# Optimization experiments

Measured on AMD Instinct MI355X. Metric: run time of the kernel, lower is better.

Reference implementation:

```python
import jax, jax.numpy as jnp
import numpy as np

MAX_LENGTH = 10
SOS = 0


def setup_inputs() -> dict:
    key = jax.random.key(0)
    ks = jax.random.split(key, 16)
    B, S, H, V = 64, 128, 1024, 32000
    sc = 0.02
    return {
        "encoder_outputs": jax.random.normal(ks[0], (B, S, H), jnp.float32),
        "encoder_hidden": jax.random.normal(ks[1], (1, B, H), jnp.float32),
        "target_tensor": jax.random.randint(ks[2], (B, MAX_LENGTH), 0, V),
        "embedding": jax.random.normal(ks[3], (V, H), jnp.float32) * sc,
        "Wa_w": jax.random.normal(ks[4], (H, H), jnp.float32) * sc,
        "Wa_b": jnp.zeros((H,), jnp.float32),
        "Ua_w": jax.random.normal(ks[5], (H, H), jnp.float32) * sc,
        "Ua_b": jnp.zeros((H,), jnp.float32),
        "Va_w": jax.random.normal(ks[6], (1, H), jnp.float32) * sc,
        "Va_b": jnp.zeros((1,), jnp.float32),
        "gru_wi": jax.random.normal(ks[7], (3 * H, 2 * H), jnp.float32) * sc,
        "gru_wh": jax.random.normal(ks[8], (3 * H, H), jnp.float32) * sc,
        "gru_bi": jnp.zeros((3 * H,), jnp.float32),
        "gru_bh": jnp.zeros((3 * H,), jnp.float32),
        "out_w": jax.random.normal(ks[9], (V, H), jnp.float32) * sc,
        "out_b": jnp.zeros((V,), jnp.float32),
    }


def reference(encoder_outputs, encoder_hidden, target_tensor, embedding,
              Wa_w, Wa_b, Ua_w, Ua_b, Va_w, Va_b,
              gru_wi, gru_wh, gru_bi, gru_bh, out_w, out_b):
    B, S, H = encoder_outputs.shape
    # teacher-forced input tokens: [SOS, tgt_0, ..., tgt_{T-2}]
    tokens = jnp.concatenate(
        [jnp.full((B, 1), SOS, dtype=target_tensor.dtype),
         target_tensor[:, :MAX_LENGTH - 1]], axis=1)  # [B, T]
    emb_seq = embedding[tokens]                         # [B, T, H] (dropout = identity)
    # precompute Ua(keys), shared across steps
    Ua_keys = jnp.einsum('bsh,kh->bsk', encoder_outputs, Ua_w) + Ua_b  # [B,S,H]
    va = Va_w[0]

    def step(h, emb_t):  # h: [B,H], emb_t: [B,H]
        q = h @ Wa_w.T + Wa_b                                   # [B,H]
        scores = jnp.einsum('bsh,h->bs', jnp.tanh(q[:, None, :] + Ua_keys), va) + Va_b[0]
        w = jax.nn.softmax(scores, axis=-1)                     # [B,S]
        ctx = jnp.einsum('bs,bsh->bh', w, encoder_outputs)      # [B,H]
        x = jnp.concatenate([emb_t, ctx], axis=-1)              # [B,2H]
        gi = x @ gru_wi.T + gru_bi                              # [B,3H]
        gh = h @ gru_wh.T + gru_bh
        r = jax.nn.sigmoid(gi[:, :H] + gh[:, :H])
        z = jax.nn.sigmoid(gi[:, H:2 * H] + gh[:, H:2 * H])
        n = jnp.tanh(gi[:, 2 * H:] + r * gh[:, 2 * H:])
        h_new = (1.0 - z) * n + z * h
        return h_new, (h_new, w)

    h0 = encoder_hidden[0]  # [B,H]
    h_final, (outs, attns) = jax.lax.scan(step, h0, jnp.swapaxes(emb_seq, 0, 1))
    outs = jnp.swapaxes(outs, 0, 1)                 # [B,T,H]
    attns = jnp.swapaxes(attns, 0, 1)               # [B,T,S]
    logits = jnp.einsum('bth,vh->btv', outs, out_w) + out_b
    log_probs = jax.nn.log_softmax(logits, axis=-1)  # [B,T,V]
    return log_probs, h_final[None], attns
```

## Files before the change

### kernel.cpp

```cpp
#include <hip/hip_runtime.h>
#include <hip/hip_bf16.h>
#include <cstddef>

#define B 64
#define S 128
#define H 1024
#define V 32000
#define T 10
#define H3 3072
#define NCHUNK 250

typedef __bf16 bf16x8 __attribute__((ext_vector_type(8)));
typedef float f32x4 __attribute__((ext_vector_type(4)));
typedef unsigned short ushort8v __attribute__((ext_vector_type(8)));

__device__ inline unsigned short f2b(float f) {
    __hip_bfloat16 h = __float2bfloat16(f);
    return *reinterpret_cast<unsigned short*>(&h);
}
__device__ inline float b2f(unsigned short u) {
    return __uint_as_float(((unsigned)u) << 16);
}
__device__ inline float fast_tanh(float x) {
    float e = __expf(2.f * x);
    return 1.f - 2.f * __builtin_amdgcn_rcpf(e + 1.f);
}
__device__ inline float fast_sigmoid(float x) {
    return __builtin_amdgcn_rcpf(1.f + __expf(-x));
}

__device__ inline void gload_lds16(const void* g, void* l) {
    __builtin_amdgcn_global_load_lds(
        (const __attribute__((address_space(1))) void*)g,
        (__attribute__((address_space(3))) void*)l, 16, 0, 0);
}

__device__ inline int xcd_swz(int orig, int nwg) {
    int q = nwg >> 3, r = nwg & 7;
    int xcd = orig & 7, idx = orig >> 3;
    int base = (xcd < r) ? xcd * (q + 1) : r * (q + 1) + (xcd - r) * q;
    return base + idx;
}

#define PREP_NB 20240
__global__ void prep_kernel(const float* __restrict__ enc, unsigned short* __restrict__ enc_bf,
                            const float* __restrict__ Ua_w, unsigned short* __restrict__ Ua_bf,
                            const float* __restrict__ gwh, const float* __restrict__ Wa_w,
                            unsigned short* __restrict__ Wcat,
                            const float* __restrict__ gwi,
                            unsigned short* __restrict__ Wemb, unsigned short* __restrict__ Wctx,
                            const float* __restrict__ gbh, const float* __restrict__ Wa_b,
                            float* __restrict__ catbias,
                            const float* __restrict__ emb, const int* __restrict__ tgt,
                            unsigned short* __restrict__ embg,
                            const float* __restrict__ h0, unsigned short* __restrict__ hbf,
                            float* __restrict__ hbuf) {
    const int bid = blockIdx.x, tid = threadIdx.x;
    if (bid < 8192) {
        int i = bid * 256 + tid;
        float4 v = reinterpret_cast<const float4*>(enc)[i];
        ushort4 o = { f2b(v.x), f2b(v.y), f2b(v.z), f2b(v.w) };
        reinterpret_cast<ushort4*>(enc_bf)[i] = o;
    } else if (bid < 9216) {
        int i = (bid - 8192) * 256 + tid;
        float4 v = reinterpret_cast<const float4*>(Ua_w)[i];
        ushort4 o = { f2b(v.x), f2b(v.y), f2b(v.z), f2b(v.w) };
        reinterpret_cast<ushort4*>(Ua_bf)[i] = o;
    } else if (bid < 13312) {
        int i = (bid - 9216) * 256 + tid;
        int e = i * 4, n = e >> 10, k = e & 1023;
        const float* src = (n < H3) ? (gwh + (size_t)n * H + k) : (Wa_w + (size_t)(n - H3) * H + k);
        float4 v = *reinterpret_cast<const float4*>(src);
        ushort4 o = { f2b(v.x), f2b(v.y), f2b(v.z), f2b(v.w) };
        reinterpret_cast<ushort4*>(Wcat)[i] = o;
    } else if (bid < 16384) {
        int i = (bid - 13312) * 256 + tid;
        int e = i * 4, n = e >> 10, k = e & 1023;
        float4 v = *reinterpret_cast<const float4*>(gwi + (size_t)n * 2 * H + k);
        ushort4 o = { f2b(v.x), f2b(v.y), f2b(v.z), f2b(v.w) };
        reinterpret_cast<ushort4*>(Wemb)[i] = o;
    } else if (bid < 19456) {
        int i = (bid - 16384) * 256 + tid;
        int e = i * 4, n = e >> 10, k = e & 1023;
        float4 v = *reinterpret_cast<const float4*>(gwi + (size_t)n * 2 * H + H + k);
        ushort4 o = { f2b(v.x), f2b(v.y), f2b(v.z), f2b(v.w) };
        reinterpret_cast<ushort4*>(Wctx)[i] = o;
    } else if (bid < 19472) {
        int n = (bid - 19456) * 256 + tid;
        catbias[n] = (n < H3) ? gbh[n] : Wa_b[n - H3];
    } else if (bid < 20112) {
        int i = (bid - 19472) * 256 + tid;
        int e = i * 4;
        int t = e >> 16, rem = e & 65535;
        int b = rem >> 10, j = rem & 1023;
        int tok = (t == 0) ? 0 : tgt[b * T + (t - 1)];
        float4 v = *reinterpret_cast<const float4*>(emb + (size_t)tok * H + j);
        ushort4 o = { f2b(v.x), f2b(v.y), f2b(v.z), f2b(v.w) };
        *reinterpret_cast<ushort4*>(embg + ((size_t)t * B + b) * H + j) = o;
    } else if (bid < 20176) {
        int i = (bid - 20112) * 256 + tid;
        float4 v = reinterpret_cast<const float4*>(h0)[i];
        ushort4 o = { f2b(v.x), f2b(v.y), f2b(v.z), f2b(v.w) };
        reinterpret_cast<ushort4*>(hbf)[i] = o;
    } else {
        int i = (bid - 20176) * 256 + tid;
        reinterpret_cast<float4*>(hbuf)[i] = reinterpret_cast<const float4*>(h0)[i];
    }
}

struct GemmDesc {
    const unsigned short* A;
    const unsigned short* Bw;
    const float* bias;
    void* C;
    int M, N, out_bf16;
};

__global__ __launch_bounds__(512) void gemm3_kernel(GemmDesc d0, GemmDesc d1, GemmDesc d2,
                                                    const float* __restrict__ out_w,
                                                    unsigned short* __restrict__ outw_bf) {
    __shared__ unsigned short As[128 * 32];
    __shared__ unsigned short Bs[128 * 32];
    const int bid = blockIdx.x;
    const int tid = threadIdx.x;
    if (bid >= 2168) {
        int i = (bid - 2168) * 512 + tid;
        float4 v = reinterpret_cast<const float4*>(out_w)[i];
        ushort4 o = { f2b(v.x), f2b(v.y), f2b(v.z), f2b(v.w) };
        reinterpret_cast<ushort4*>(outw_bf)[i] = o;
        return;
    }
    GemmDesc d; int local, nwg;
    if (bid < 512)       { d = d0; local = bid;        nwg = 512;  }
    else if (bid < 2048) { d = d1; local = bid - 512;  nwg = 1536; }
    else                 { d = d2; local = bid - 2048; nwg = 120;  }
    local = xcd_swz(local, nwg);
    const int mtiles = d.M >> 7;
    const int bm = (local % mtiles) << 7, bn = (local / mtiles) << 7;
    const int lane = tid & 63, w = tid >> 6;
    const int wm = w >> 2, wn = w & 3;
    const int quad = lane >> 4, fr = lane & 15;
    const int K = H;
    f32x4 acc[4][2] = {};

    const int sr = w * 16 + (lane >> 2), sc = (lane & 3) * 8;
    const unsigned short* agp = d.A + (size_t)(bm + sr) * K + sc;
    const unsigned short* bgp = d.Bw + (size_t)(bn + sr) * K + sc;
    unsigned short* alp = As + w * 512;
    unsigned short* blp = Bs + w * 512;

    for (int k0 = 0; k0 < K; k0 += 32) {
        gload_lds16(agp + k0, alp);
        gload_lds16(bgp + k0, blp);
        __syncthreads();
        const int kg = quad * 8;
        bf16x8 a[4], bb[2];
        #pragma unroll
        for (int m = 0; m < 4; ++m)
            a[m] = *reinterpret_cast<const bf16x8*>(&As[(64 * wm + 16 * m + fr) * 32 + kg]);
        #pragma unroll
        for (int n = 0; n < 2; ++n)
            bb[n] = *reinterpret_cast<const bf16x8*>(&Bs[(32 * wn + 16 * n + fr) * 32 + kg]);
        #pragma unroll
        for (int m = 0; m < 4; ++m)
            #pragma unroll
            for (int n = 0; n < 2; ++n)
                acc[m][n] = __builtin_amdgcn_mfma_f32_16x16x32_bf16(a[m], bb[n], acc[m][n], 0, 0, 0);
        __syncthreads();
    }
    #pragma unroll
    for (int n = 0; n < 2; ++n) {
        int col = bn + 32 * wn + 16 * n + fr;
        float bv = d.bias ? d.bias[col] : 0.f;
        #pragma unroll
        for (int m = 0; m < 4; ++m)
            #pragma unroll
            for (int i = 0; i < 4; ++i) {
                int row = bm + 64 * wm + 16 * m + quad * 4 + i;
                float v = acc[m][n][i] + bv;
                if (d.out_bf16)
                    ((unsigned short*)d.C)[(size_t)row * d.N + col] = f2b(v);
                else
                    ((float*)d.C)[(size_t)row * d.N + col] = v;
            }
    }
}

__global__ __launch_bounds__(512) void gemm_logits(const unsigned short* __restrict__ A,
                                                   const unsigned short* __restrict__ Bw,
                                                   const float* __restrict__ bias,
                                                   float* __restrict__ Cout,
                                                   float2* __restrict__ stats,
                                                   int M, int N, int K) {
    __shared__ unsigned short As[128 * 32];
    __shared__ unsigned short Bs[128 * 32];
    __shared__ float mred[128][4];
    __shared__ float sred[128][4];
    const int wg = xcd_swz(blockIdx.x, gridDim.x);
    const int mtiles = M >> 7;
    const int bm = (wg % mtiles) << 7, bn = (wg / mtiles) << 7;
    const int tid = threadIdx.x, lane = tid & 63, w = tid >> 6;
    const int wm = w >> 2, wn = w & 3;
    const int quad = lane >> 4, fr = lane & 15;
    f32x4 acc[4][2] = {};

    const int sr = w * 16 + (lane >> 2), sc = (lane & 3) * 8;
    const unsigned short* agp = A + (size_t)(bm + sr) * K + sc;
    const unsigned short* bgp = Bw + (size_t)(bn + sr) * K + sc;
    unsigned short* alp = As + w * 512;
    unsigned short* blp = Bs + w * 512;

    for (int k0 = 0; k0 < K; k0 += 32) {
        gload_lds16(agp + k0, alp);
        gload_lds16(bgp + k0, blp);
        __syncthreads();
        const int kg = quad * 8;
        bf16x8 a[4], bb[2];
        #pragma unroll
        for (int m = 0; m < 4; ++m)
            a[m] = *reinterpret_cast<const bf16x8*>(&As[(64 * wm + 16 * m + fr) * 32 + kg]);
        #pragma unroll
        for (int n = 0; n < 2; ++n)
            bb[n] = *reinterpret_cast<const bf16x8*>(&Bs[(32 * wn + 16 * n + fr) * 32 + kg]);
        #pragma unroll
        for (int m = 0; m < 4; ++m)
            #pragma unroll
            for (int n = 0; n < 2; ++n)
                acc[m][n] = __builtin_amdgcn_mfma_f32_16x16x32_bf16(a[m], bb[n], acc[m][n], 0, 0, 0);
        __syncthreads();
    }

    #pragma unroll
    for (int n = 0; n < 2; ++n) {
        int col = bn + 32 * wn + 16 * n + fr;
        float bv = bias[col];
        #pragma unroll
        for (int m = 0; m < 4; ++m)
            #pragma unroll
            for (int i = 0; i < 4; ++i) {
                int row = bm + 64 * wm + 16 * m + quad * 4 + i;
                float v = acc[m][n][i] + bv;
                Cout[(size_t)row * N + col] = v;
                acc[m][n][i] = v;
            }
    }

    const int nchunk = N >> 7;
    #pragma unroll
    for (int m = 0; m < 4; ++m)
        #pragma unroll
        for (int i = 0; i < 4; ++i) {
            float x = fmaxf(acc[m][0][i], acc[m][1][i]);
            x = fmaxf(x, __shfl_xor(x, 1)); x = fmaxf(x, __shfl_xor(x, 2));
            x = fmaxf(x, __shfl_xor(x, 4)); x = fmaxf(x, __shfl_xor(x, 8));
            if (fr == 0) mred[64 * wm + 16 * m + quad * 4 + i][wn] = x;
        }
    __syncthreads();
    #pragma unroll
    for (int m = 0; m < 4; ++m)
        #pragma unroll
        for (int i = 0; i < 4; ++i) {
            int rl = 64 * wm + 16 * m + quad * 4 + i;
            float Mr = fmaxf(fmaxf(mred[rl][0], mred[rl][1]), fmaxf(mred[rl][2], mred[rl][3]));
            float sv = expf(acc[m][0][i] - Mr) + expf(acc[m][1][i] - Mr);
            sv += __shfl_xor(sv, 1); sv += __shfl_xor(sv, 2);
            sv += __shfl_xor(sv, 4); sv += __shfl_xor(sv, 8);
            if (fr == 0) sred[rl][wn] = sv;
        }
    __syncthreads();
    if (tid < 128) {
        float Mr = fmaxf(fmaxf(mred[tid][0], mred[tid][1]), fmaxf(mred[tid][2], mred[tid][3]));
        float Sv = sred[tid][0] + sred[tid][1] + sred[tid][2] + sred[tid][3];
        stats[(size_t)(bm + tid) * nchunk + (bn >> 7)] = make_float2(Mr, Sv);
    }
}

__global__ __launch_bounds__(256) void gemm_smallA(const unsigned short* __restrict__ A,
                                                   const unsigned short* __restrict__ Bw,
                                                   const float* __restrict__ bias,
                                                   float* __restrict__ Cout) {
    __shared__ unsigned short As[64][136];
    __shared__ unsigned short Bs[32][136];
    const int bn = blockIdx.x * 32;
    const int tid = threadIdx.x, lane = tid & 63, w = tid >> 6;
    const int quad = lane >> 4, fr = lane & 15;
    f32x4 acc[2] = {};

    const int srA = tid >> 2, scA = (tid & 3) * 32;
    const int srB = tid >> 3, scB = (tid & 7) * 16;
    for (int k0 = 0; k0 < H; k0 += 128) {
        const unsigned short* ap = A + (size_t)srA * H + k0 + scA;
        #pragma unroll
        for (int u = 0; u < 4; ++u)
            *reinterpret_cast<bf16x8*>(&As[srA][scA + 8 * u]) =
                *reinterpret_cast<const bf16x8*>(ap + 8 * u);
        const unsigned short* bp = Bw + (size_t)(bn + srB) * H + k0 + scB;
        *reinterpret_cast<bf16x8*>(&Bs[srB][scB])     = *reinterpret_cast<const bf16x8*>(bp);
        *reinterpret_cast<bf16x8*>(&Bs[srB][scB + 8]) = *reinterpret_cast<const bf16x8*>(bp + 8);
        __syncthreads();
        #pragma unroll
        for (int ks = 0; ks < 4; ++ks) {
            const int kg = quad * 8 + 32 * ks;
            bf16x8 a = *reinterpret_cast<const bf16x8*>(&As[16 * w + fr][kg]);
            #pragma unroll
            for (int n = 0; n < 2; ++n) {
                bf16x8 bb = *reinterpret_cast<const bf16x8*>(&Bs[16 * n + fr][kg]);
                acc[n] = __builtin_amdgcn_mfma_f32_16x16x32_bf16(a, bb, acc[n], 0, 0, 0);
            }
        }
        __syncthreads();
    }
    #pragma unroll
    for (int n = 0; n < 2; ++n) {
        int col = bn + 16 * n + fr;
        float bv = bias[col];
        #pragma unroll
        for (int i = 0; i < 4; ++i) {
            int row = 16 * w + quad * 4 + i;
            Cout[(size_t)row * 4096 + col] = acc[n][i] + bv;
        }
    }
}

__global__ __launch_bounds__(256) void stepB(const float* __restrict__ ghq,
                                             const unsigned short* __restrict__ keys,
                                             const unsigned short* __restrict__ KV,
                                             const float* __restrict__ va,
                                             const float* __restrict__ va_b,
                                             const float* __restrict__ gi_emb,
                                             float* __restrict__ h,
                                             unsigned short* __restrict__ hbf,
                                             unsigned short* __restrict__ outs_bf,
                                             float* __restrict__ attns,
                                             float* __restrict__ h_final, int t) {
    const int q = blockIdx.x, b = blockIdx.y;
    const int tid = threadIdx.x, lane = tid & 63, wv = tid >> 6;
    __shared__ float ssc[128];
    __shared__ float sw[128];
    __shared__ float red[4][64][13];

    float qv[16], vv[16];
    {
        const float* qp = ghq + (size_t)b * 4096 + H3 + lane * 16;
        const float* vp = va + lane * 16;
        #pragma unroll
        for (int j = 0; j < 16; ++j) { qv[j] = qp[j]; vv[j] = vp[j]; }
    }
    const float vab = va_b[0];
    const unsigned short* kb = keys + (size_t)b * S * H;
    for (int i = 0; i < 32; i += 2) {
        int s0 = wv * 32 + i;
        const unsigned short* kr0 = kb + (size_t)s0 * H + lane * 16;
        const unsigned short* kr1 = kr0 + H;
        ushort8v k00 = *reinterpret_cast<const ushort8v*>(kr0);
        ushort8v k01 = *reinterpret_cast<const ushort8v*>(kr0 + 8);
        ushort8v k10 = *reinterpret_cast<const ushort8v*>(kr1);
        ushort8v k11 = *reinterpret_cast<const ushort8v*>(kr1 + 8);
        float a0 = 0.f, a1 = 0.f;
        #pragma unroll
        for (int e = 0; e < 8; ++e) {
            a0 += fast_tanh(qv[e] + b2f(k00[e])) * vv[e];
            a1 += fast_tanh(qv[e] + b2f(k10[e])) * vv[e];
        }
        #pragma unroll
        for (int e = 0; e < 8; ++e) {
            a0 += fast_tanh(qv[8 + e] + b2f(k01[e])) * vv[8 + e];
            a1 += fast_tanh(qv[8 + e] + b2f(k11[e])) * vv[8 + e];
        }
        a0 += __shfl_xor(a0, 1);  a1 += __shfl_xor(a1, 1);
        a0 += __shfl_xor(a0, 2);  a1 += __shfl_xor(a1, 2);
        a0 += __shfl_xor(a0, 4);  a1 += __shfl_xor(a1, 4);
        a0 += __shfl_xor(a0, 8);  a1 += __shfl_xor(a1, 8);
        a0 += __shfl_xor(a0, 16); a1 += __shfl_xor(a1, 16);
        a0 += __shfl_xor(a0, 32); a1 += __shfl_xor(a1, 32);
        if (lane == 0) { ssc[s0] = a0 + vab; ssc[s0 + 1] = a1 + vab; }
    }
    __syncthreads();
    if (tid < 128) {
        float mx = -1e30f;
        #pragma unroll 8
        for (int s = 0; s < 128; ++s) mx = fmaxf(mx, ssc[s]);
        float sum = 0.f;
        #pragma unroll 8
        for (int s = 0; s < 128; ++s) sum += __expf(ssc[s] - mx);
        float wvv = __expf(ssc[tid] - mx) / sum;
        sw[tid] = wvv;
        if (q == 0) attns[((size_t)b * T + t) * S + tid] = wvv;
    }
    __syncthreads();

    const int j0 = q * 256 + lane * 4;
    float ar[4] = {}, az[4] = {}, an[4] = {};
    const unsigned short* kvb = KV + (size_t)b * S * H3 + j0;
    for (int i = 0; i < 32; i += 2) {
        int s0 = wv * 32 + i;
        float w0 = sw[s0], w1 = sw[s0 + 1];
        const unsigned short* r0 = kvb + (size_t)s0 * H3;
        const unsigned short* r1 = r0 + H3;
        uint2 u0a = *reinterpret_cast<const uint2*>(r0);
        uint2 u1a = *reinterpret_cast<const uint2*>(r0 + 1024);
        uint2 u2a = *reinterpret_cast<const uint2*>(r0 + 2048);
        uint2 u0b = *reinterpret_cast<const uint2*>(r1);
        uint2 u1b = *reinterpret_cast<const uint2*>(r1 + 1024);
        uint2 u2b = *reinterpret_cast<const uint2*>(r1 + 2048);
        ar[0] += w0 * b2f((unsigned short)(u0a.x & 0xffff)) + w1 * b2f((unsigned short)(u0b.x & 0xffff));
        ar[1] += w0 * b2f((unsigned short)(u0a.x >> 16))    + w1 * b2f((unsigned short)(u0b.x >> 16));
        ar[2] += w0 * b2f((unsigned short)(u0a.y & 0xffff)) + w1 * b2f((unsigned short)(u0b.y & 0xffff));
        ar[3] += w0 * b2f((unsigned short)(u0a.y >> 16))    + w1 * b2f((unsigned short)(u0b.y >> 16));
        az[0] += w0 * b2f((unsigned short)(u1a.x & 0xffff)) + w1 * b2f((unsigned short)(u1b.x & 0xffff));
        az[1] += w0 * b2f((unsigned short)(u1a.x >> 16))    + w1 * b2f((unsigned short)(u1b.x >> 16));
        az[2] += w0 * b2f((unsigned short)(u1a.y & 0xffff)) + w1 * b2f((unsigned short)(u1b.y & 0xffff));
        az[3] += w0 * b2f((unsigned short)(u1a.y >> 16))    + w1 * b2f((unsigned short)(u1b.y >> 16));
        an[0] += w0 * b2f((unsigned short)(u2a.x & 0xffff)) + w1 * b2f((unsigned short)(u2b.x & 0xffff));
        an[1] += w0 * b2f((unsigned short)(u2a.x >> 16))    + w1 * b2f((unsigned short)(u2b.x >> 16));
        an[2] += w0 * b2f((unsigned short)(u2a.y & 0xffff)) + w1 * b2f((unsigned short)(u2b.y & 0xffff));
        an[3] += w0 * b2f((unsigned short)(u2a.y >> 16))    + w1 * b2f((unsigned short)(u2b.y >> 16));
    }
    #pragma unroll
    for (int g = 0; g < 4; ++g) {
        red[wv][lane][g]     = ar[g];
        red[wv][lane][4 + g] = az[g];
        red[wv][lane][8 + g] = an[g];
    }
    __syncthreads();

    if (tid < 64) {
        float rr[4], zz[4], nn[4];
        #pragma unroll
        for (int g = 0; g < 4; ++g) {
            rr[g] = red[0][tid][g] + red[1][tid][g] + red[2][tid][g] + red[3][tid][g];
            zz[g] = red[0][tid][4+g] + red[1][tid][4+g] + red[2][tid][4+g] + red[3][tid][4+g];
            nn[g] = red[0][tid][8+g] + red[1][tid][8+g] + red[2][tid][8+g] + red[3][tid][8+g];
        }
        const int jj = q * 256 + tid * 4;
        const float* ge = gi_emb + ((size_t)t * B + b) * H3;
        const float* gh = ghq + (size_t)b * 4096;
        float geR[4], geZ[4], geN[4], ghR[4], ghZ[4], ghN[4], hv[4];
        *reinterpret_cast<float4*>(geR) = *reinterpret_cast<const float4*>(ge + jj);
        *reinterpret_cast<float4*>(geZ) = *reinterpret_cast<const float4*>(ge + 1024 + jj);
        *reinterpret_cast<float4*>(geN) = *reinterpret_cast<const float4*>(ge + 2048 + jj);
        *reinterpret_cast<float4*>(ghR) = *reinterpret_cast<const float4*>(gh + jj);
        *reinterpret_cast<float4*>(ghZ) = *reinterpret_cast<const float4*>(gh + 1024 + jj);
        *reinterpret_cast<float4*>(ghN) = *reinterpret_cast<const float4*>(gh + 2048 + jj);
        *reinterpret_cast<float4*>(hv)  = *reinterpret_cast<const float4*>(h + (size_t)b * H + jj);
        ushort4 hb;
        unsigned short* hbp = reinterpret_cast<unsigned short*>(&hb);
        #pragma unroll
        for (int i = 0; i < 4; ++i) {
            float r = fast_sigmoid(geR[i] + rr[i] + ghR[i]);
            float z = fast_sigmoid(geZ[i] + zz[i] + ghZ[i]);
            float n = fast_tanh(geN[i] + nn[i] + r * ghN[i]);
            hv[i] = (1.f - z) * n + z * hv[i];
            hbp[i] = f2b(hv[i]);
        }
        *reinterpret_cast<float4*>(h + (size_t)b * H + jj) = *reinterpret_cast<float4*>(hv);
        *reinterpret_cast<ushort4*>(hbf + (size_t)b * H + jj) = hb;
        *reinterpret_cast<ushort4*>(outs_bf + ((size_t)b * T + t) * H + jj) = hb;
        if (t == T - 1)
            *reinterpret_cast<float4*>(h_final + (size_t)b * H + jj) = *reinterpret_cast<float4*>(hv);
    }
}

__global__ void lsesub_kernel(const float2* __restrict__ stats, float* __restrict__ x) {
    const int row = blockIdx.x;
    const int tid = threadIdx.x;
    __shared__ float shm[256];
    __shared__ float shs[256];
    float mv = -1e30f, sv = 0.f;
    float2 st = make_float2(-1e30f, 0.f);
    if (tid < NCHUNK) { st = stats[(size_t)row * NCHUNK + tid]; mv = st.x; }
    shm[tid] = mv; __syncthreads();
    for (int off = 128; off > 0; off >>= 1) {
        if (tid < off) shm[tid] = fmaxf(shm[tid], shm[tid + off]);
        __syncthreads();
    }
    float M = shm[0]; __syncthreads();
    if (tid < NCHUNK) sv = st.y * expf(st.x - M);
    shs[tid] = sv; __syncthreads();
    for (int off = 128; off > 0; off >>= 1) {
        if (tid < off) shs[tid] += shs[tid + off];
        __syncthreads();
    }
    float L = M + logf(shs[0]);
    __syncthreads();
    float4* p = reinterpret_cast<float4*>(x + (size_t)row * V);
    for (int i = tid; i < V / 4; i += 256) {
        float4 v = p[i];
        v.x -= L; v.y -= L; v.z -= L; v.w -= L;
        p[i] = v;
    }
}


extern "C" void kernel_launch(void* const* d_in, const int* in_sizes, int n_in,
                              void* d_out, int out_size, void* d_ws, size_t ws_size,
                              hipStream_t stream) {
    const float* enc   = (const float*)d_in[0];
    const float* h0    = (const float*)d_in[1];
    const int*   tgt   = (const int*)d_in[2];
    const float* emb   = (const float*)d_in[3];
    const float* Wa_w  = (const float*)d_in[4];
    const float* Wa_b  = (const float*)d_in[5];
    const float* Ua_w  = (const float*)d_in[6];
    const float* Ua_b  = (const float*)d_in[7];
    const float* Va_w  = (const float*)d_in[8];
    const float* Va_b  = (const float*)d_in[9];
    const float* gwi   = (const float*)d_in[10];
    const float* gwh   = (const float*)d_in[11];
    const float* gbi   = (const float*)d_in[12];
    const float* gbh   = (const float*)d_in[13];
    const float* out_w = (const float*)d_in[14];
    const float* out_b = (const float*)d_in[15];

    float* out       = (float*)d_out;
    float* log_probs = out;
    float* h_final   = out + (size_t)B * T * V;
    float* attns     = h_final + (size_t)B * H;

    char* pp = (char*)d_ws;
    auto alloc = [&](size_t bytes) { char* r = pp; pp += (bytes + 255) & ~(size_t)255; return r; };
    unsigned short* ua_bf   = (unsigned short*)alloc((size_t)B * S * H * 2);
    unsigned short* enc_bf  = (unsigned short*)alloc((size_t)B * S * H * 2);
    unsigned short* outw_bf = (unsigned short*)alloc((size_t)V * H * 2);
    unsigned short* KV      = (unsigned short*)alloc((size_t)B * S * H3 * 2);
    unsigned short* Ua_bf   = (unsigned short*)alloc((size_t)H * H * 2);
    unsigned short* Wcat    = (unsigned short*)alloc((size_t)4096 * H * 2);
    unsigned short* Wctx    = (unsigned short*)alloc((size_t)H3 * H * 2);
    unsigned short* Wemb    = (unsigned short*)alloc((size_t)H3 * H * 2);
    float*          catbias = (float*)alloc(4096 * 4);
    unsigned short* embg    = (unsigned short*)alloc((size_t)T * B * H * 2);
    float*          gi_emb  = (float*)alloc((size_t)T * B * H3 * 4);
    float*          hbuf    = (float*)alloc((size_t)B * H * 4);
    unsigned short* hbf     = (unsigned short*)alloc((size_t)B * H * 2);
    float*          ghq     = (float*)alloc((size_t)B * 4096 * 4);
    unsigned short* outs_bf = (unsigned short*)alloc((size_t)B * T * H * 2);
    float2*         stats   = (float2*)alloc((size_t)B * T * NCHUNK * 8);

    prep_kernel<<<PREP_NB, 256, 0, stream>>>(enc, enc_bf, Ua_w, Ua_bf,
                                             gwh, Wa_w, Wcat, gwi, Wemb, Wctx,
                                             gbh, Wa_b, catbias, emb, tgt, embg,
                                             h0, hbf, hbuf);

    GemmDesc d0 = { enc_bf, Ua_bf, Ua_b, (void*)ua_bf,  B * S, H,  1 };
    GemmDesc d1 = { enc_bf, Wctx,  nullptr, (void*)KV,  B * S, H3, 1 };
    GemmDesc d2 = { embg,   Wemb,  gbi, (void*)gi_emb,  T * B, H3, 0 };
    gemm3_kernel<<<18168, 512, 0, stream>>>(d0, d1, d2, out_w, outw_bf);

    for (int t = 0; t < T; ++t) {
        gemm_smallA<<<128, 256, 0, stream>>>(hbf, Wcat, catbias, ghq);
        stepB<<<dim3(4, B), 256, 0, stream>>>(ghq, ua_bf, KV, Va_w, Va_b, gi_emb,
                                              hbuf, hbf, outs_bf, attns, h_final, t);
    }

    gemm_logits<<<(B * T / 128) * (V / 128), 512, 0, stream>>>(
        outs_bf, outw_bf, out_b, log_probs, stats, B * T, V, H);
    lsesub_kernel<<<B * T, 256, 0, stream>>>(stats, log_probs);
}
```

Before: 712.3 us.

## Fuse per-step GEMM and attention/GRU kernels with atomic-counter grid handoff

Merges the small hidden-state GEMM and the attention/GRU step into one launch per timestep. The first 128 blocks compute ghq and bump per-group atomic counters. The remaining 256 blocks spin on a completion counter before reading ghq. This removes one kernel launch and its inter-kernel gap per step, at the cost of spin-waiting and relying on all blocks being co-resident. It also adds a memset of the per-step counters.

```diff
diff --git a/kernel.cpp b/kernel.cpp
--- a/kernel.cpp
+++ b/kernel.cpp
@@ -275,70 +275,85 @@
     }
 }
 
-__global__ __launch_bounds__(256) void gemm_smallA(const unsigned short* __restrict__ A,
-                                                   const unsigned short* __restrict__ Bw,
-                                                   const float* __restrict__ bias,
-                                                   float* __restrict__ Cout) {
-    __shared__ unsigned short As[64][136];
-    __shared__ unsigned short Bs[32][136];
-    const int bn = blockIdx.x * 32;
-    const int tid = threadIdx.x, lane = tid & 63, w = tid >> 6;
+__global__ __launch_bounds__(256) void step_kernel(const unsigned short* __restrict__ hbf_in,
+                                                   const unsigned short* __restrict__ Wcat,
+                                                   const float* __restrict__ catbias,
+                                                   float* __restrict__ ghq,
+                                                   const unsigned short* __restrict__ keys,
+                                                   const unsigned short* __restrict__ KV,
+                                                   const float* __restrict__ va,
+                                                   const float* __restrict__ va_b,
+                                                   const float* __restrict__ gi_emb,
+                                                   float* __restrict__ h,
+                                                   unsigned short* __restrict__ hbf_out,
+                                                   unsigned short* __restrict__ outs_bf,
+                                                   float* __restrict__ attns,
+                                                   float* __restrict__ h_final,
+                                                   unsigned int* __restrict__ ctr, int t) {
+    const int bid = blockIdx.x;
+    const int tid = threadIdx.x, lane = tid & 63, wv = tid >> 6;
     const int quad = lane >> 4, fr = lane & 15;
-    f32x4 acc[2] = {};
-
-    const int srA = tid >> 2, scA = (tid & 3) * 32;
-    const int srB = tid >> 3, scB = (tid & 7) * 16;
-    for (int k0 = 0; k0 < H; k0 += 128) {
-        const unsigned short* ap = A + (size_t)srA * H + k0 + scA;
-        #pragma unroll
-        for (int u = 0; u < 4; ++u)
-            *reinterpret_cast<bf16x8*>(&As[srA][scA + 8 * u]) =
-                *reinterpret_cast<const bf16x8*>(ap + 8 * u);
-        const unsigned short* bp = Bw + (size_t)(bn + srB) * H + k0 + scB;
-        *reinterpret_cast<bf16x8*>(&Bs[srB][scB])     = *reinterpret_cast<const bf16x8*>(bp);
-        *reinterpret_cast<bf16x8*>(&Bs[srB][scB + 8]) = *reinterpret_cast<const bf16x8*>(bp + 8);
-        __syncthreads();
-        #pragma unroll
-        for (int ks = 0; ks < 4; ++ks) {
-            const int kg = quad * 8 + 32 * ks;
-            bf16x8 a = *reinterpret_cast<const bf16x8*>(&As[16 * w + fr][kg]);
-            #pragma unroll
-            for (int n = 0; n < 2; ++n) {
-                bf16x8 bb = *reinterpret_cast<const bf16x8*>(&Bs[16 * n + fr][kg]);
-                acc[n] = __builtin_amdgcn_mfma_f32_16x16x32_bf16(a, bb, acc[n], 0, 0, 0);
+
+    if (bid < 128) {
+        __shared__ unsigned short As[64][136];
+        __shared__ unsigned short Bs[32][136];
+        const int bn = bid * 32;
+        f32x4 acc[2] = {};
+        const int srA = tid >> 2, scA = (tid & 3) * 32;
+        const int srB = tid >> 3, scB = (tid & 7) * 16;
+        for (int k0 = 0; k0 < H; k0 += 128) {
+            const unsigned short* ap = hbf_in + (size_t)srA * H + k0 + scA;
+            #pragma unroll
+            for (int u = 0; u < 4; ++u)
+                *reinterpret_cast<bf16x8*>(&As[srA][scA + 8 * u]) =
+                    *reinterpret_cast<const bf16x8*>(ap + 8 * u);
+            const unsigned short* bp = Wcat + (size_t)(bn + srB) * H + k0 + scB;
+            *reinterpret_cast<bf16x8*>(&Bs[srB][scB])     = *reinterpret_cast<const bf16x8*>(bp);
+            *reinterpret_cast<bf16x8*>(&Bs[srB][scB + 8]) = *reinterpret_cast<const bf16x8*>(bp + 8);
+            __syncthreads();
+            #pragma unroll
+            for (int ks = 0; ks < 4; ++ks) {
+                const int kg = quad * 8 + 32 * ks;
+                bf16x8 a = *reinterpret_cast<const bf16x8*>(&As[16 * wv + fr][kg]);
+                #pragma unroll
+                for (int n = 0; n < 2; ++n) {
+                    bf16x8 bb = *reinterpret_cast<const bf16x8*>(&Bs[16 * n + fr][kg]);
+                    acc[n] = __builtin_amdgcn_mfma_f32_16x16x32_bf16(a, bb, acc[n], 0, 0, 0);
+                }
             }
-        }
-        __syncthreads();
-    }
-    #pragma unroll
-    for (int n = 0; n < 2; ++n) {
-        int col = bn + 16 * n + fr;
-        float bv = bias[col];
-        #pragma unroll
-        for (int i = 0; i < 4; ++i) {
-            int row = 16 * w + quad * 4 + i;
-            Cout[(size_t)row * 4096 + col] = acc[n][i] + bv;
-        }
-    }
-}
-
-__global__ __launch_bounds__(256) void stepB(const float* __restrict__ ghq,
-                                             const unsigned short* __restrict__ keys,
-                                             const unsigned short* __restrict__ KV,
-                                             const float* __restrict__ va,
-                                             const float* __restrict__ va_b,
-                                             const float* __restrict__ gi_emb,
-                                             float* __restrict__ h,
-                                             unsigned short* __restrict__ hbf,
-                                             unsigned short* __restrict__ outs_bf,
-                                             float* __restrict__ attns,
-                                             float* __restrict__ h_final, int t) {
-    const int q = blockIdx.x, b = blockIdx.y;
-    const int tid = threadIdx.x, lane = tid & 63, wv = tid >> 6;
+            __syncthreads();
+        }
+        #pragma unroll
+        for (int n = 0; n < 2; ++n) {
+            int col = bn + 16 * n + fr;
+            float bv = catbias[col];
+            #pragma unroll
+            for (int i = 0; i < 4; ++i) {
+                int row = 16 * wv + quad * 4 + i;
+                ghq[(size_t)row * 4096 + col] = acc[n][i] + bv;
+            }
+        }
+        __syncthreads();
+        if (tid == 0) {
+            __threadfence();
+            unsigned old = atomicAdd(&ctr[(bid >> 5) * 32], 1u);
+            if (old == 31u) atomicAdd(&ctr[4 * 32], 1u);
+        }
+        return;
+    }
+
     __shared__ float ssc[128];
     __shared__ float sw[128];
     __shared__ float red[4][64][13];
-
+    if (tid == 0) {
+        while (__hip_atomic_load(&ctr[4 * 32], __ATOMIC_RELAXED, __HIP_MEMORY_SCOPE_AGENT) < 4u)
+            __builtin_amdgcn_s_sleep(2);
+        __builtin_amdgcn_fence(__ATOMIC_ACQUIRE, "agent");
+    }
+    __syncthreads();
+
+    const int bid2 = bid - 128;
+    const int q = bid2 & 3, b = bid2 >> 2;
     float qv[16], vv[16];
     {
         const float* qp = ghq + (size_t)b * 4096 + H3 + lane * 16;
@@ -454,7 +469,7 @@
             hbp[i] = f2b(hv[i]);
         }
         *reinterpret_cast<float4*>(h + (size_t)b * H + jj) = *reinterpret_cast<float4*>(hv);
-        *reinterpret_cast<ushort4*>(hbf + (size_t)b * H + jj) = hb;
+        *reinterpret_cast<ushort4*>(hbf_out + (size_t)b * H + jj) = hb;
         *reinterpret_cast<ushort4*>(outs_bf + ((size_t)b * T + t) * H + jj) = hb;
         if (t == T - 1)
             *reinterpret_cast<float4*>(h_final + (size_t)b * H + jj) = *reinterpret_cast<float4*>(hv);
@@ -535,6 +550,9 @@
     float*          ghq     = (float*)alloc((size_t)B * 4096 * 4);
     unsigned short* outs_bf = (unsigned short*)alloc((size_t)B * T * H * 2);
     float2*         stats   = (float2*)alloc((size_t)B * T * NCHUNK * 8);
+    unsigned int*   ctrs    = (unsigned int*)alloc((size_t)T * 5 * 32 * 4);
+
+    hipMemsetAsync(ctrs, 0, (size_t)T * 5 * 32 * 4, stream);
 
     prep_kernel<<<PREP_NB, 256, 0, stream>>>(enc, enc_bf, Ua_w, Ua_bf,
                                              gwh, Wa_w, Wcat, gwi, Wemb, Wctx,
@@ -547,9 +565,9 @@
     gemm3_kernel<<<18168, 512, 0, stream>>>(d0, d1, d2, out_w, outw_bf);
 
     for (int t = 0; t < T; ++t) {
-        gemm_smallA<<<128, 256, 0, stream>>>(hbf, Wcat, catbias, ghq);
-        stepB<<<dim3(4, B), 256, 0, stream>>>(ghq, ua_bf, KV, Va_w, Va_b, gi_emb,
-                                              hbuf, hbf, outs_bf, attns, h_final, t);
+        step_kernel<<<384, 256, 0, stream>>>(hbf, Wcat, catbias, ghq, ua_bf, KV,
+                                             Va_w, Va_b, gi_emb, hbuf, hbf, outs_bf,
+                                             attns, h_final, ctrs + (size_t)t * 5 * 32, t);
     }
 
     gemm_logits<<<(B * T / 128) * (V / 128), 512, 0, stream>>>(
```

Result: slower. 780.2 us (+9.5%).

## Fuse fp32-to-bf16 conversion into precompute GEMM loads and drop prep kernel

Applied to the files above, without the earlier changes.

Removes the separate prep kernel that converted encoder outputs and weights to bf16. The precompute GEMMs now read fp32 operands directly, convert them in registers, and store them to LDS. The embedding gather is folded into the A-row addressing, and the remaining small conversions move into spare blocks of the GEMM launch. The GEMM K-step also doubles to 64 using two LDS buffers, halving barrier count. This saves one launch and the bf16 intermediate round-trips through memory. The cost is fp32 global loads, which are twice as wide, plus conversion work inside the GEMM, and the direct global-to-LDS path is dropped for this kernel.

```diff
diff --git a/kernel.cpp b/kernel.cpp
--- a/kernel.cpp
+++ b/kernel.cpp
@@ -42,94 +42,71 @@
     return base + idx;
 }
 
-#define PREP_NB 20240
-__global__ void prep_kernel(const float* __restrict__ enc, unsigned short* __restrict__ enc_bf,
-                            const float* __restrict__ Ua_w, unsigned short* __restrict__ Ua_bf,
-                            const float* __restrict__ gwh, const float* __restrict__ Wa_w,
-                            unsigned short* __restrict__ Wcat,
-                            const float* __restrict__ gwi,
-                            unsigned short* __restrict__ Wemb, unsigned short* __restrict__ Wctx,
-                            const float* __restrict__ gbh, const float* __restrict__ Wa_b,
-                            float* __restrict__ catbias,
-                            const float* __restrict__ emb, const int* __restrict__ tgt,
-                            unsigned short* __restrict__ embg,
-                            const float* __restrict__ h0, unsigned short* __restrict__ hbf,
-                            float* __restrict__ hbuf) {
-    const int bid = blockIdx.x, tid = threadIdx.x;
-    if (bid < 8192) {
-        int i = bid * 256 + tid;
-        float4 v = reinterpret_cast<const float4*>(enc)[i];
-        ushort4 o = { f2b(v.x), f2b(v.y), f2b(v.z), f2b(v.w) };
-        reinterpret_cast<ushort4*>(enc_bf)[i] = o;
-    } else if (bid < 9216) {
-        int i = (bid - 8192) * 256 + tid;
-        float4 v = reinterpret_cast<const float4*>(Ua_w)[i];
-        ushort4 o = { f2b(v.x), f2b(v.y), f2b(v.z), f2b(v.w) };
-        reinterpret_cast<ushort4*>(Ua_bf)[i] = o;
-    } else if (bid < 13312) {
-        int i = (bid - 9216) * 256 + tid;
-        int e = i * 4, n = e >> 10, k = e & 1023;
-        const float* src = (n < H3) ? (gwh + (size_t)n * H + k) : (Wa_w + (size_t)(n - H3) * H + k);
-        float4 v = *reinterpret_cast<const float4*>(src);
-        ushort4 o = { f2b(v.x), f2b(v.y), f2b(v.z), f2b(v.w) };
-        reinterpret_cast<ushort4*>(Wcat)[i] = o;
-    } else if (bid < 16384) {
-        int i = (bid - 13312) * 256 + tid;
-        int e = i * 4, n = e >> 10, k = e & 1023;
-        float4 v = *reinterpret_cast<const float4*>(gwi + (size_t)n * 2 * H + k);
-        ushort4 o = { f2b(v.x), f2b(v.y), f2b(v.z), f2b(v.w) };
-        reinterpret_cast<ushort4*>(Wemb)[i] = o;
-    } else if (bid < 19456) {
-        int i = (bid - 16384) * 256 + tid;
-        int e = i * 4, n = e >> 10, k = e & 1023;
-        float4 v = *reinterpret_cast<const float4*>(gwi + (size_t)n * 2 * H + H + k);
-        ushort4 o = { f2b(v.x), f2b(v.y), f2b(v.z), f2b(v.w) };
-        reinterpret_cast<ushort4*>(Wctx)[i] = o;
-    } else if (bid < 19472) {
-        int n = (bid - 19456) * 256 + tid;
-        catbias[n] = (n < H3) ? gbh[n] : Wa_b[n - H3];
-    } else if (bid < 20112) {
-        int i = (bid - 19472) * 256 + tid;
-        int e = i * 4;
-        int t = e >> 16, rem = e & 65535;
-        int b = rem >> 10, j = rem & 1023;
-        int tok = (t == 0) ? 0 : tgt[b * T + (t - 1)];
-        float4 v = *reinterpret_cast<const float4*>(emb + (size_t)tok * H + j);
-        ushort4 o = { f2b(v.x), f2b(v.y), f2b(v.z), f2b(v.w) };
-        *reinterpret_cast<ushort4*>(embg + ((size_t)t * B + b) * H + j) = o;
-    } else if (bid < 20176) {
-        int i = (bid - 20112) * 256 + tid;
-        float4 v = reinterpret_cast<const float4*>(h0)[i];
-        ushort4 o = { f2b(v.x), f2b(v.y), f2b(v.z), f2b(v.w) };
-        reinterpret_cast<ushort4*>(hbf)[i] = o;
-    } else {
-        int i = (bid - 20176) * 256 + tid;
-        reinterpret_cast<float4*>(hbuf)[i] = reinterpret_cast<const float4*>(h0)[i];
-    }
-}
-
+__device__ inline ushort8v cvt8(const float* p) {
+    float4 f0 = *reinterpret_cast<const float4*>(p);
+    float4 f1 = *reinterpret_cast<const float4*>(p + 4);
+    ushort8v u;
+    u[0] = f2b(f0.x); u[1] = f2b(f0.y); u[2] = f2b(f0.z); u[3] = f2b(f0.w);
+    u[4] = f2b(f1.x); u[5] = f2b(f1.y); u[6] = f2b(f1.z); u[7] = f2b(f1.w);
+    return u;
+}
+
+#define G3_NB 20288
 struct GemmDesc {
-    const unsigned short* A;
-    const unsigned short* Bw;
+    const float* A;
+    const float* Bw;
     const float* bias;
     void* C;
-    int M, N, out_bf16;
+    int M, N;
+    int brstride, bcoff;
+    int out_bf16, gatherA;
 };
 
 __global__ __launch_bounds__(512) void gemm3_kernel(GemmDesc d0, GemmDesc d1, GemmDesc d2,
+                                                    const int* __restrict__ tgt,
                                                     const float* __restrict__ out_w,
-                                                    unsigned short* __restrict__ outw_bf) {
-    __shared__ unsigned short As[128 * 32];
-    __shared__ unsigned short Bs[128 * 32];
+                                                    unsigned short* __restrict__ outw_bf,
+                                                    const float* __restrict__ gwh,
+                                                    const float* __restrict__ Wa_w,
+                                                    unsigned short* __restrict__ Wcat,
+                                                    const float* __restrict__ gbh,
+                                                    const float* __restrict__ Wa_b,
+                                                    float* __restrict__ catbias,
+                                                    const float* __restrict__ h0,
+                                                    unsigned short* __restrict__ hbf,
+                                                    float* __restrict__ hbuf) {
     const int bid = blockIdx.x;
     const int tid = threadIdx.x;
     if (bid >= 2168) {
-        int i = (bid - 2168) * 512 + tid;
-        float4 v = reinterpret_cast<const float4*>(out_w)[i];
-        ushort4 o = { f2b(v.x), f2b(v.y), f2b(v.z), f2b(v.w) };
-        reinterpret_cast<ushort4*>(outw_bf)[i] = o;
+        if (bid < 18168) {
+            int i = (bid - 2168) * 512 + tid;
+            float4 v = reinterpret_cast<const float4*>(out_w)[i];
+            ushort4 o = { f2b(v.x), f2b(v.y), f2b(v.z), f2b(v.w) };
+            reinterpret_cast<ushort4*>(outw_bf)[i] = o;
+        } else if (bid < 20216) {
+            int i = (bid - 18168) * 512 + tid;
+            int e = i * 4, n = e >> 10, k = e & 1023;
+            const float* src = (n < H3) ? (gwh + (size_t)n * H + k) : (Wa_w + (size_t)(n - H3) * H + k);
+            float4 v = *reinterpret_cast<const float4*>(src);
+            ushort4 o = { f2b(v.x), f2b(v.y), f2b(v.z), f2b(v.w) };
+            reinterpret_cast<ushort4*>(Wcat)[i] = o;
+        } else if (bid < 20224) {
+            int n = (bid - 20216) * 512 + tid;
+            catbias[n] = (n < H3) ? gbh[n] : Wa_b[n - H3];
+        } else if (bid < 20256) {
+            int i = (bid - 20224) * 512 + tid;
+            float4 v = reinterpret_cast<const float4*>(h0)[i];
+            ushort4 o = { f2b(v.x), f2b(v.y), f2b(v.z), f2b(v.w) };
+            reinterpret_cast<ushort4*>(hbf)[i] = o;
+        } else {
+            int i = (bid - 20256) * 512 + tid;
+            reinterpret_cast<float4*>(hbuf)[i] = reinterpret_cast<const float4*>(h0)[i];
+        }
         return;
     }
+
+    __shared__ unsigned short As0[128 * 32], As1[128 * 32];
+    __shared__ unsigned short Bs0[128 * 32], Bs1[128 * 32];
     GemmDesc d; int local, nwg;
     if (bid < 512)       { d = d0; local = bid;        nwg = 512;  }
     else if (bid < 2048) { d = d1; local = bid - 512;  nwg = 1536; }
@@ -140,32 +117,53 @@
     const int lane = tid & 63, w = tid >> 6;
     const int wm = w >> 2, wn = w & 3;
     const int quad = lane >> 4, fr = lane & 15;
-    const int K = H;
     f32x4 acc[4][2] = {};
 
-    const int sr = w * 16 + (lane >> 2), sc = (lane & 3) * 8;
-    const unsigned short* agp = d.A + (size_t)(bm + sr) * K + sc;
-    const unsigned short* bgp = d.Bw + (size_t)(bn + sr) * K + sc;
-    unsigned short* alp = As + w * 512;
-    unsigned short* blp = Bs + w * 512;
-
-    for (int k0 = 0; k0 < K; k0 += 32) {
-        gload_lds16(agp + k0, alp);
-        gload_lds16(bgp + k0, blp);
-        __syncthreads();
-        const int kg = quad * 8;
-        bf16x8 a[4], bb[2];
-        #pragma unroll
-        for (int m = 0; m < 4; ++m)
-            a[m] = *reinterpret_cast<const bf16x8*>(&As[(64 * wm + 16 * m + fr) * 32 + kg]);
-        #pragma unroll
-        for (int n = 0; n < 2; ++n)
-            bb[n] = *reinterpret_cast<const bf16x8*>(&Bs[(32 * wn + 16 * n + fr) * 32 + kg]);
-        #pragma unroll
-        for (int m = 0; m < 4; ++m)
+    const int sr = tid >> 2, q4 = tid & 3;
+    const int ck = q4 >> 1, cc = (q4 & 1) * 16;
+    const int gcol = ck * 32 + cc;
+    unsigned short* asel = (ck ? As1 : As0) + sr * 32 + cc;
+    unsigned short* bsel = (ck ? Bs1 : Bs0) + sr * 32 + cc;
+
+    const float* arow;
+    if (d.gatherA) {
+        int m = bm + sr;
+        int tt = m >> 6, bb = m & 63;
+        int tok = (tt == 0) ? 0 : tgt[bb * T + tt - 1];
+        arow = d.A + (size_t)tok * H;
+    } else {
+        arow = d.A + (size_t)(bm + sr) * H;
+    }
+    const float* brow = d.Bw + (size_t)(bn + sr) * d.brstride + d.bcoff;
+
+    for (int k0 = 0; k0 < H; k0 += 64) {
+        ushort8v ua0 = cvt8(arow + k0 + gcol);
+        ushort8v ua1 = cvt8(arow + k0 + gcol + 8);
+        ushort8v ub0 = cvt8(brow + k0 + gcol);
+        ushort8v ub1 = cvt8(brow + k0 + gcol + 8);
+        *reinterpret_cast<ushort8v*>(asel)     = ua0;
+        *reinterpret_cast<ushort8v*>(asel + 8) = ua1;
+        *reinterpret_cast<ushort8v*>(bsel)     = ub0;
+        *reinterpret_cast<ushort8v*>(bsel + 8) = ub1;
+        __syncthreads();
+        #pragma unroll
+        for (int ks = 0; ks < 2; ++ks) {
+            const unsigned short* Asrc = ks ? As1 : As0;
+            const unsigned short* Bsrc = ks ? Bs1 : Bs0;
+            const int kg = quad * 8;
+            bf16x8 a[4], bb[2];
+            #pragma unroll
+            for (int m = 0; m < 4; ++m)
+                a[m] = *reinterpret_cast<const bf16x8*>(&Asrc[(64 * wm + 16 * m + fr) * 32 + kg]);
             #pragma unroll
             for (int n = 0; n < 2; ++n)
-                acc[m][n] = __builtin_amdgcn_mfma_f32_16x16x32_bf16(a[m], bb[n], acc[m][n], 0, 0, 0);
+                bb[n] = *reinterpret_cast<const bf16x8*>(&Bsrc[(32 * wn + 16 * n + fr) * 32 + kg]);
+            #pragma unroll
+            for (int m = 0; m < 4; ++m)
+                #pragma unroll
+                for (int n = 0; n < 2; ++n)
+                    acc[m][n] = __builtin_amdgcn_mfma_f32_16x16x32_bf16(a[m], bb[n], acc[m][n], 0, 0, 0);
+        }
         __syncthreads();
     }
     #pragma unroll
@@ -192,8 +190,8 @@
                                                    float* __restrict__ Cout,
                                                    float2* __restrict__ stats,
                                                    int M, int N, int K) {
-    __shared__ unsigned short As[128 * 32];
-    __shared__ unsigned short Bs[128 * 32];
+    __shared__ unsigned short As0[128 * 32], As1[128 * 32];
+    __shared__ unsigned short Bs0[128 * 32], Bs1[128 * 32];
     __shared__ float mred[128][4];
     __shared__ float sred[128][4];
     const int wg = xcd_swz(blockIdx.x, gridDim.x);
@@ -207,26 +205,35 @@
     const int sr = w * 16 + (lane >> 2), sc = (lane & 3) * 8;
     const unsigned short* agp = A + (size_t)(bm + sr) * K + sc;
     const unsigned short* bgp = Bw + (size_t)(bn + sr) * K + sc;
-    unsigned short* alp = As + w * 512;
-    unsigned short* blp = Bs + w * 512;
-
-    for (int k0 = 0; k0 < K; k0 += 32) {
-        gload_lds16(agp + k0, alp);
-        gload_lds16(bgp + k0, blp);
-        __syncthreads();
-        const int kg = quad * 8;
-        bf16x8 a[4], bb[2];
-        #pragma unroll
-        for (int m = 0; m < 4; ++m)
-            a[m] = *reinterpret_cast<const bf16x8*>(&As[(64 * wm + 16 * m + fr) * 32 + kg]);
-        #pragma unroll
-        for (int n = 0; n < 2; ++n)
-            bb[n] = *reinterpret_cast<const bf16x8*>(&Bs[(32 * wn + 16 * n + fr) * 32 + kg]);
-        #pragma unroll
-        for (int m = 0; m < 4; ++m)
+    unsigned short* a0 = As0 + w * 512;
+    unsigned short* a1 = As1 + w * 512;
+    unsigned short* b0 = Bs0 + w * 512;
+    unsigned short* b1 = Bs1 + w * 512;
+
+    for (int k0 = 0; k0 < K; k0 += 64) {
+        gload_lds16(agp + k0, a0);
+        gload_lds16(agp + k0 + 32, a1);
+        gload_lds16(bgp + k0, b0);
+        gload_lds16(bgp + k0 + 32, b1);
+        __syncthreads();
+        #pragma unroll
+        for (int ks = 0; ks < 2; ++ks) {
+            const unsigned short* Asrc = ks ? As1 : As0;
+            const unsigned short* Bsrc = ks ? Bs1 : Bs0;
+            const int kg = quad * 8;
+            bf16x8 a[4], bb[2];
+            #pragma unroll
+            for (int m = 0; m < 4; ++m)
+                a[m] = *reinterpret_cast<const bf16x8*>(&Asrc[(64 * wm + 16 * m + fr) * 32 + kg]);
             #pragma unroll
             for (int n = 0; n < 2; ++n)
-                acc[m][n] = __builtin_amdgcn_mfma_f32_16x16x32_bf16(a[m], bb[n], acc[m][n], 0, 0, 0);
+                bb[n] = *reinterpret_cast<const bf16x8*>(&Bsrc[(32 * wn + 16 * n + fr) * 32 + kg]);
+            #pragma unroll
+            for (int m = 0; m < 4; ++m)
+                #pragma unroll
+                for (int n = 0; n < 2; ++n)
+                    acc[m][n] = __builtin_amdgcn_mfma_f32_16x16x32_bf16(a[m], bb[n], acc[m][n], 0, 0, 0);
+        }
         __syncthreads();
     }
 
@@ -520,15 +527,10 @@
     char* pp = (char*)d_ws;
     auto alloc = [&](size_t bytes) { char* r = pp; pp += (bytes + 255) & ~(size_t)255; return r; };
     unsigned short* ua_bf   = (unsigned short*)alloc((size_t)B * S * H * 2);
-    unsigned short* enc_bf  = (unsigned short*)alloc((size_t)B * S * H * 2);
     unsigned short* outw_bf = (unsigned short*)alloc((size_t)V * H * 2);
     unsigned short* KV      = (unsigned short*)alloc((size_t)B * S * H3 * 2);
-    unsigned short* Ua_bf   = (unsigned short*)alloc((size_t)H * H * 2);
     unsigned short* Wcat    = (unsigned short*)alloc((size_t)4096 * H * 2);
-    unsigned short* Wctx    = (unsigned short*)alloc((size_t)H3 * H * 2);
-    unsigned short* Wemb    = (unsigned short*)alloc((size_t)H3 * H * 2);
     float*          catbias = (float*)alloc(4096 * 4);
-    unsigned short* embg    = (unsigned short*)alloc((size_t)T * B * H * 2);
     float*          gi_emb  = (float*)alloc((size_t)T * B * H3 * 4);
     float*          hbuf    = (float*)alloc((size_t)B * H * 4);
     unsigned short* hbf     = (unsigned short*)alloc((size_t)B * H * 2);
@@ -536,15 +538,12 @@
     unsigned short* outs_bf = (unsigned short*)alloc((size_t)B * T * H * 2);
     float2*         stats   = (float2*)alloc((size_t)B * T * NCHUNK * 8);
 
-    prep_kernel<<<PREP_NB, 256, 0, stream>>>(enc, enc_bf, Ua_w, Ua_bf,
-                                             gwh, Wa_w, Wcat, gwi, Wemb, Wctx,
-                                             gbh, Wa_b, catbias, emb, tgt, embg,
-                                             h0, hbf, hbuf);
-
-    GemmDesc d0 = { enc_bf, Ua_bf, Ua_b, (void*)ua_bf,  B * S, H,  1 };
-    GemmDesc d1 = { enc_bf, Wctx,  nullptr, (void*)KV,  B * S, H3, 1 };
-    GemmDesc d2 = { embg,   Wemb,  gbi, (void*)gi_emb,  T * B, H3, 0 };
-    gemm3_kernel<<<18168, 512, 0, stream>>>(d0, d1, d2, out_w, outw_bf);
+    GemmDesc d0 = { enc, Ua_w, Ua_b, (void*)ua_bf,  B * S, H,  H,     0, 1, 0 };
+    GemmDesc d1 = { enc, gwi,  nullptr, (void*)KV,  B * S, H3, 2 * H, H, 1, 0 };
+    GemmDesc d2 = { emb, gwi,  gbi, (void*)gi_emb,  T * B, H3, 2 * H, 0, 0, 1 };
+    gemm3_kernel<<<G3_NB, 512, 0, stream>>>(d0, d1, d2, tgt, out_w, outw_bf,
+                                            gwh, Wa_w, Wcat, gbh, Wa_b, catbias,
+                                            h0, hbf, hbuf);
 
     for (int t = 0; t < T; ++t) {
         gemm_smallA<<<128, 256, 0, stream>>>(hbf, Wcat, catbias, ghq);
```

New measurement: 808.6 us. +13.5%, slower.
